# Performance work log

Measured on AMD Instinct MI355X. Metric: run time of the kernel, lower is better.

The kernel has to match this reference:

```python
import jax, jax.numpy as jnp
import numpy as np
from jax import lax

N_FEAT = 150          # feature-map side
N_AR = 9              # anchors per cell
PRE_NMS = 6000        # mode='test'
POST_NMS = 300        # mode='test'
IOU_TH = 0.7
MIN_SIZE = 16.0 / 1000.0


def _make_anchors():
    # grid of centers in [0,1], 9 anchors per cell (3 scales x 3 ratios), xyxy form
    cs = (np.arange(N_FEAT) + 0.5) / N_FEAT
    cy, cx = np.meshgrid(cs, cs, indexing='ij')
    scales = np.array([0.05, 0.1, 0.2])
    ratios = np.array([0.5, 1.0, 2.0])
    ws = (scales[:, None] * np.sqrt(ratios)[None, :]).reshape(-1)  # [9]
    hs = (scales[:, None] / np.sqrt(ratios)[None, :]).reshape(-1)
    cx = np.repeat(cx.reshape(-1), N_AR)
    cy = np.repeat(cy.reshape(-1), N_AR)
    ws = np.tile(ws, N_FEAT * N_FEAT)
    hs = np.tile(hs, N_FEAT * N_FEAT)
    xy = np.stack([cx - ws / 2, cy - hs / 2, cx + ws / 2, cy + hs / 2], axis=-1)
    return xy.astype(np.float32)  # [N,4]


def xy_to_cxcy(xy):
    return jnp.concatenate([(xy[:, 2:] + xy[:, :2]) / 2, xy[:, 2:] - xy[:, :2]], axis=-1)


def cxcy_to_xy(cxcy):
    return jnp.concatenate([cxcy[:, :2] - cxcy[:, 2:] / 2, cxcy[:, :2] + cxcy[:, 2:] / 2], axis=-1)


def decode(t, priors_cxcy):
    cxcy = t[:, :2] * priors_cxcy[:, 2:] + priors_cxcy[:, :2]
    wh = jnp.exp(t[:, 2:]) * priors_cxcy[:, 2:]
    return jnp.concatenate([cxcy, wh], axis=-1)


def pairwise_iou(b):
    # b: [K,4] xyxy -> [K,K]
    area = (b[:, 2] - b[:, 0]) * (b[:, 3] - b[:, 1])
    lt = jnp.maximum(b[:, None, :2], b[None, :, :2])
    rb = jnp.minimum(b[:, None, 2:], b[None, :, 2:])
    wh = jnp.clip(rb - lt, 0.0)
    inter = wh[..., 0] * wh[..., 1]
    return inter / (area[:, None] + area[None, :] - inter + 1e-12)


def greedy_nms_mask(boxes, valid):
    # boxes sorted by score desc; returns bool keep mask of shape [K]
    K = boxes.shape[0]
    iou = pairwise_iou(boxes)  # [K,K]  (~144 MB for K=6000)
    idx = jnp.arange(K)

    def body(i, keep):
        active = keep[i] & valid[i]
        supp = (iou[i] > IOU_TH) & (idx > i) & active
        return keep & ~supp

    keep = lax.fori_loop(0, K, body, jnp.ones(K, dtype=bool))
    return keep & valid


def setup_inputs() -> dict:
    key = jax.random.key(0)
    k1, k2 = jax.random.split(key)
    N = N_FEAT * N_FEAT * N_AR
    pred_cls = jax.random.normal(k1, (1, N, 2), dtype=jnp.float32)
    pred_loc = jax.random.normal(k2, (1, N, 4), dtype=jnp.float32) * 0.1
    anchor = jnp.asarray(_make_anchors())
    return {"pred_cls": pred_cls, "pred_loc": pred_loc, "anchor": anchor}


def reference(pred_cls, pred_loc, anchor):
    # squeeze batch dim of 1
    scores = jax.nn.softmax(pred_cls[0], axis=-1)[:, 1]  # [N] objectness
    priors = xy_to_cxcy(anchor)
    roi = jnp.clip(cxcy_to_xy(decode(pred_loc[0], priors)), 0.0, 1.0)  # [N,4]

    ws = roi[:, 2] - roi[:, 0]
    hs = roi[:, 3] - roi[:, 1]
    valid = (ws >= MIN_SIZE) & (hs >= MIN_SIZE)

    # size filter via masking (scores in [0,1], so -1 sorts below all valid)
    scores_m = jnp.where(valid, scores, -1.0)
    top_scores, top_idx = lax.top_k(scores_m, PRE_NMS)
    boxes = roi[top_idx]           # [PRE_NMS,4], score-descending
    valid_k = top_scores >= 0.0

    keep = greedy_nms_mask(boxes, valid_k)  # [PRE_NMS] bool

    # gather kept boxes in score order, take first POST_NMS, zero-pad the rest
    order = jnp.argsort(jnp.where(keep, jnp.arange(PRE_NMS), PRE_NMS))
    sel = order[:POST_NMS]
    out = boxes[sel] * keep[sel][:, None].astype(boxes.dtype)  # [POST_NMS,4]
    return out
```

## Files before the change

### kernel.cpp

```cpp
#include <hip/hip_runtime.h>
#include <hip/hip_bf16.h>

#define NANCH 202500
#define PRE_NMS 6000
#define POST_NMS 300
#define KW 94
#define CAP 8192
#define NBUCK 16384
#define BSHIFT 18
#define IOU_TH 0.7f
#define MIN_SIZE 0.016f
#define TB_PAD 6016
#define RTILE 256
#define RITEMS 8
#define SBLK 256
#define CBLK 198

typedef unsigned long long ull;

__device__ inline float4 decode_box(const float* __restrict__ loc,
                                    const float* __restrict__ anc, int i) {
    float4 a = ((const float4*)anc)[i];
    float4 t = ((const float4*)loc)[i];
    float pw = a.z - a.x, ph = a.w - a.y;
    float pcx = (a.x + a.z) * 0.5f, pcy = (a.y + a.w) * 0.5f;
    float cx = t.x * pw + pcx, cy = t.y * ph + pcy;
    float w = expf(t.z) * pw, h = expf(t.w) * ph;
    float x1 = fminf(fmaxf(cx - 0.5f * w, 0.f), 1.f);
    float y1 = fminf(fmaxf(cy - 0.5f * h, 0.f), 1.f);
    float x2 = fminf(fmaxf(cx + 0.5f * w, 0.f), 1.f);
    float y2 = fminf(fmaxf(cy + 0.5f * h, 0.f), 1.f);
    return make_float4(x1, y1, x2, y2);
}

__device__ inline unsigned make_key(const float* __restrict__ cls,
                                    const float* __restrict__ loc,
                                    const float* __restrict__ anc, int i) {
    float2 c = ((const float2*)cls)[i];
    float d = c.y - c.x;
    float4 b = decode_box(loc, anc, i);
    bool valid = ((b.z - b.x) >= MIN_SIZE) && ((b.w - b.y) >= MIN_SIZE);
    unsigned ib = __float_as_uint(d);
    unsigned u = (ib & 0x80000000u) ? ~ib : (ib | 0x80000000u);
    return valid ? u : 0u;
}

__device__ inline ull orx64(ull v, int m) {
    unsigned lo = (unsigned)v, hi = (unsigned)(v >> 32);
    lo = (unsigned)__shfl_xor((int)lo, m, 64);
    hi = (unsigned)__shfl_xor((int)hi, m, 64);
    return ((ull)hi << 32) | lo;
}

__device__ inline bool iou_gt(float4 bi, float4 bj, float ai) {
    float aj = (bj.z - bj.x) * (bj.w - bj.y);
    float lx = fmaxf(bi.x, bj.x), ly = fmaxf(bi.y, bj.y);
    float rx = fminf(bi.z, bj.z), ry = fminf(bi.w, bj.w);
    float iw = fmaxf(rx - lx, 0.f), ih = fmaxf(ry - ly, 0.f);
    float inter = iw * ih;
    return inter > IOU_TH * (ai + aj - inter);
}

__global__ __launch_bounds__(256) void k_score(const float* __restrict__ cls,
                                               const float* __restrict__ loc,
                                               const float* __restrict__ anc,
                                               unsigned* __restrict__ hist,
                                               unsigned* __restrict__ keyc, int n) {
    __shared__ unsigned lh[NBUCK];
    int tid = threadIdx.x, bid = blockIdx.x;
    for (int q = tid; q < NBUCK; q += 256) lh[q] = 0u;
    __syncthreads();
    for (int i = bid * 256 + tid; i < n; i += SBLK * 256) {
        unsigned u = make_key(cls, loc, anc, i);
        if (keyc) keyc[i] = u;
        atomicAdd(&lh[u >> BSHIFT], 1u);
    }
    __syncthreads();
    for (int qq = 0; qq < NBUCK / 256; qq++) {
        int q = (qq + bid) & (NBUCK / 256 - 1);
        int b = q * 256 + tid;
        unsigned v = lh[b];
        if (v) atomicAdd(&hist[b], v);
    }
}

__global__ __launch_bounds__(256) void k_compactB(const unsigned* __restrict__ keyc,
                                                  const unsigned* __restrict__ hist,
                                                  unsigned* __restrict__ meta,
                                                  ull* __restrict__ cand, int n) {
    __shared__ unsigned ps[256];
    __shared__ unsigned Bs;
    __shared__ unsigned wbase[5];
    int tid = threadIdx.x, bid = blockIdx.x;
    const uint4* h4 = (const uint4*)hist;
    unsigned local = 0;
    #pragma unroll
    for (int b = 0; b < 16; b++) {
        uint4 v = h4[tid * 16 + b];
        local += v.x + v.y + v.z + v.w;
    }
    ps[tid] = local;
    __syncthreads();
    for (int off = 1; off < 256; off <<= 1) {
        unsigned add = (tid + off < 256) ? ps[tid + off] : 0u;
        __syncthreads();
        ps[tid] += add;
        __syncthreads();
    }
    unsigned incl = ps[tid];
    unsigned excl = incl - local;
    if (incl >= (unsigned)PRE_NMS && excl < (unsigned)PRE_NMS) {
        unsigned hv[64];
        #pragma unroll
        for (int b = 0; b < 16; b++) {
            uint4 v = h4[tid * 16 + b];
            hv[4 * b] = v.x; hv[4 * b + 1] = v.y;
            hv[4 * b + 2] = v.z; hv[4 * b + 3] = v.w;
        }
        unsigned cum = excl;
        int B = tid * 64;
        for (int b = 63; b >= 0; b--) {
            cum += hv[b];
            if (cum >= (unsigned)PRE_NMS) { B = tid * 64 + b; break; }
        }
        Bs = (unsigned)B;
    }
    __syncthreads();
    unsigned B = Bs;
    int lane = tid & 63, wv = tid >> 6;
    unsigned uk[4]; bool pr[4]; unsigned lpre[4], kpre[4];
    ull ltm = (1ull << lane) - 1ull;
    unsigned wsum = 0;
    #pragma unroll
    for (int k = 0; k < 4; k++) {
        int i = bid * 1024 + k * 256 + tid;
        unsigned u = (i < n) ? keyc[i] : 0u;
        uk[k] = u;
        bool pred = (i < n) && ((u >> BSHIFT) >= B);
        pr[k] = pred;
        ull m = __ballot(pred);
        lpre[k] = (unsigned)__popcll(m & ltm);
        kpre[k] = wsum;
        wsum += (unsigned)__popcll(m);
    }
    if (lane == 0) wbase[wv] = wsum;
    __syncthreads();
    if (tid == 0) {
        unsigned s = 0;
        #pragma unroll
        for (int w = 0; w < 4; w++) { unsigned t = wbase[w]; wbase[w] = s; s += t; }
        wbase[4] = atomicAdd(&meta[1], s);
    }
    __syncthreads();
    unsigned base = wbase[4] + wbase[wv];
    #pragma unroll
    for (int k = 0; k < 4; k++) {
        if (pr[k]) {
            unsigned p = base + kpre[k] + lpre[k];
            if (p < CAP)
                cand[p] = ((ull)(~uk[k]) << 32) | (unsigned)(bid * 1024 + k * 256 + tid);
        }
    }
}

__global__ __launch_bounds__(256) void k_ranksc(const ull* __restrict__ cand,
                                                const unsigned* __restrict__ meta,
                                                const float* __restrict__ loc,
                                                const float* __restrict__ anc,
                                                float4* __restrict__ topbox,
                                                ull* __restrict__ vmask) {
    __shared__ __align__(16) ull tile[256];
    int tid = threadIdx.x, bid = blockIdx.x;
    unsigned C = meta[1]; if (C > CAP) C = CAP;
    int sub = tid >> 3, octl = tid & 7;
    int ci = bid * 32 + sub;
    ull ki = (ci < (int)C) ? cand[ci] : 0ull;
    unsigned cnt = 0;
    int ntile = ((int)C + 255) / 256;
    for (int tt = 0; tt < ntile; tt++) {
        int j = tt * 256 + tid;
        tile[tid] = (j < (int)C) ? cand[j] : ~0ull;
        __syncthreads();
        #pragma unroll
        for (int jj = 0; jj < 32; jj++)
            cnt += (unsigned)(tile[jj * 8 + octl] < ki);
        __syncthreads();
    }
    cnt += (unsigned)__shfl_xor((int)cnt, 1, 64);
    cnt += (unsigned)__shfl_xor((int)cnt, 2, 64);
    cnt += (unsigned)__shfl_xor((int)cnt, 4, 64);
    if (octl == 0 && ci < (int)C) {
        unsigned uu = ~(unsigned)(ki >> 32);
        if (uu != 0u && cnt < (unsigned)PRE_NMS) {
            topbox[cnt] = decode_box(loc, anc, (int)(unsigned)ki);
            atomicOr(&vmask[cnt >> 6], 1ull << (cnt & 63));
        }
    }
}

__global__ __launch_bounds__(64) void k_supp(const float4* __restrict__ topbox,
                                             ull* __restrict__ supp,
                                             ull* __restrict__ sdg) {
    int cb = blockIdx.x, rb = blockIdx.y;
    if (cb < rb) return;
    int i = rb * 64 + threadIdx.x;
    __shared__ float4 cbox[64];
    int jt = cb * 64 + threadIdx.x;
    cbox[threadIdx.x] = (jt < PRE_NMS) ? topbox[jt] : make_float4(0.f, 0.f, 0.f, 0.f);
    __syncthreads();
    if (i >= PRE_NMS) return;
    float4 bi = topbox[i];
    float ai = (bi.z - bi.x) * (bi.w - bi.y);
    ull bits = 0ull;
    int j0 = cb * 64;
    for (int jj = 0; jj < 64; jj++) {
        int j = j0 + jj;
        if (j <= i || j >= PRE_NMS) continue;
        if (iou_gt(bi, cbox[jj], ai)) bits |= (1ull << jj);
    }
    supp[(size_t)i * KW + cb] = bits;
    if (cb == rb) sdg[i] = bits;
}

__global__ __launch_bounds__(64) void k_scan(const ull* __restrict__ supp,
                                             const ull* __restrict__ sdg,
                                             const ull* __restrict__ vmask,
                                             const float4* __restrict__ topbox,
                                             float* __restrict__ out) {
    __shared__ int klist[POST_NMS + 64];
    __shared__ ull vm_s[KW];
    int l = threadIdx.x;
    for (int q = l; q < KW; q += 64) vm_s[q] = vmask[q];
    __syncthreads();
    int nk = 0;
    for (int c = 0; c < KW && nk < POST_NMS; c++) {
        ull vm = vm_s[c];
        if (!vm) continue;
        int row = c * 64 + l;
        ull sd = (row < PRE_NMS) ? sdg[row] : 0ull;
        ull inc = 0ull;
        for (int q = l; q < nk; q += 64)
            inc |= supp[(size_t)klist[q] * KW + c];
        #pragma unroll
        for (int off = 32; off; off >>= 1) inc |= orx64(inc, off);
        ull todo = vm & ~inc;
        unsigned tlo = __builtin_amdgcn_readfirstlane((unsigned)todo);
        unsigned thi = __builtin_amdgcn_readfirstlane((unsigned)(todo >> 32));
        ull td = ((ull)thi << 32) | tlo;
        if (!td) continue;
        unsigned sdlo = (unsigned)sd, sdhi = (unsigned)(sd >> 32);
        ull keepw = 0ull;
        while (td) {
            int b = __builtin_ctzll(td);
            unsigned mlo = __builtin_amdgcn_readlane(sdlo, b);
            unsigned mhi = __builtin_amdgcn_readlane(sdhi, b);
            ull m = (((ull)mhi << 32) | mlo) | (1ull << b);
            keepw |= 1ull << b;
            td &= ~m;
        }
        int pos = nk + (int)__popcll(keepw & ((1ull << l) - 1ull));
        if ((keepw >> l) & 1ull) klist[pos] = row;
        nk += (int)__popcll(keepw);
        __syncthreads();
    }
    __syncthreads();
    int nout = nk < POST_NMS ? nk : POST_NMS;
    for (int q = l; q < nout; q += 64)
        ((float4*)out)[q] = topbox[klist[q]];
    for (int q = nout + l; q < POST_NMS; q += 64)
        ((float4*)out)[q] = make_float4(0.f, 0.f, 0.f, 0.f);
}

__global__ __launch_bounds__(1024) void k_findb(const unsigned* __restrict__ hist,
                                                unsigned* __restrict__ meta) {
    __shared__ unsigned ps[1024];
    int t = threadIdx.x;
    int base = t * (NBUCK / 1024);
    unsigned local = 0;
    for (int b = 0; b < NBUCK / 1024; b++) local += hist[base + b];
    ps[t] = local;
    __syncthreads();
    for (int off = 1; off < 1024; off <<= 1) {
        unsigned add = (t + off < 1024) ? ps[t + off] : 0u;
        __syncthreads();
        ps[t] += add;
        __syncthreads();
    }
    unsigned incl = ps[t];
    unsigned excl = incl - local;
    if (incl >= (unsigned)PRE_NMS && excl < (unsigned)PRE_NMS) {
        unsigned cum = excl;
        int B = base;
        for (int b = NBUCK / 1024 - 1; b >= 0; b--) {
            cum += hist[base + b];
            if (cum >= (unsigned)PRE_NMS) { B = base + b; break; }
        }
        meta[0] = (unsigned)B;
    }
}

__global__ __launch_bounds__(256) void k_compactR(const float* __restrict__ cls,
                                                  const float* __restrict__ loc,
                                                  const float* __restrict__ anc,
                                                  unsigned* __restrict__ meta,
                                                  ull* __restrict__ cand, int n) {
    int i = blockIdx.x * blockDim.x + threadIdx.x;
    if (i >= n) return;
    unsigned u = make_key(cls, loc, anc, i);
    if ((u >> BSHIFT) >= meta[0]) {
        unsigned p = atomicAdd(&meta[1], 1u);
        if (p < CAP) cand[p] = ((ull)(~u) << 32) | (unsigned)i;
    }
}

__global__ __launch_bounds__(256) void k_rank(const ull* __restrict__ cand,
                                              const unsigned* __restrict__ meta,
                                              unsigned* __restrict__ rank,
                                              float4* __restrict__ topbox) {
    __shared__ __align__(16) ull tile[RTILE];
    int tid = threadIdx.x;
    int bx = blockIdx.x, by = blockIdx.y;
    unsigned C = meta[1]; if (C > CAP) C = CAP;
    if (by == 0) {
        int per = TB_PAD / (CAP / (256 * RITEMS));
        int s0 = bx * per;
        for (int q = tid; q < per; q += 256)
            topbox[s0 + q] = make_float4(-1.f, -1.f, -1.f, -1.f);
    }
    int ibase = bx * 256 * RITEMS;
    ull ki[RITEMS]; unsigned cnt[RITEMS];
    #pragma unroll
    for (int r = 0; r < RITEMS; r++) {
        int i = ibase + r * 256 + tid;
        ki[r] = (i < (int)C) ? cand[i] : ~0ull;
        cnt[r] = 0u;
    }
    int j = by * RTILE + tid;
    tile[tid] = (j < (int)C) ? cand[j] : ~0ull;
    __syncthreads();
    const ulonglong2* t2 = (const ulonglong2*)tile;
    for (int q = 0; q < RTILE / 2; q++) {
        ulonglong2 v = t2[q];
        #pragma unroll
        for (int r = 0; r < RITEMS; r++)
            cnt[r] += (unsigned)(v.x < ki[r]) + (unsigned)(v.y < ki[r]);
    }
    #pragma unroll
    for (int r = 0; r < RITEMS; r++)
        if (cnt[r]) atomicAdd(&rank[ibase + r * 256 + tid], cnt[r]);
}

__global__ __launch_bounds__(256) void k_scatter(const ull* __restrict__ cand,
                                                 const unsigned* __restrict__ meta,
                                                 const unsigned* __restrict__ rank,
                                                 const float* __restrict__ loc,
                                                 const float* __restrict__ anc,
                                                 float4* __restrict__ topbox,
                                                 ull* __restrict__ vmask) {
    int i = blockIdx.x * 256 + threadIdx.x;
    unsigned C = meta[1]; if (C > CAP) C = CAP;
    if (i >= (int)C) return;
    ull kv = cand[i];
    unsigned uu = ~(unsigned)(kv >> 32);
    if (uu == 0u) return;
    unsigned r = rank[i];
    if (r >= PRE_NMS) return;
    int idx = (int)(unsigned)kv;
    topbox[r] = decode_box(loc, anc, idx);
    atomicOr(&vmask[r >> 6], 1ull << (r & 63));
}

__global__ __launch_bounds__(64) void k_nms(const float4* __restrict__ topbox,
                                            float* __restrict__ out) {
    int l = threadIdx.x;
    float4 kb[5];
    int nk = 0;
    for (int q0 = 0; q0 < TB_PAD && nk < POST_NMS; q0 += 64) {
        float4 myb = topbox[q0 + l];
        for (int b = 0; b < 64 && nk < POST_NMS; b++) {
            float4 bb;
            bb.x = __shfl(myb.x, b, 64);
            bb.y = __shfl(myb.y, b, 64);
            bb.z = __shfl(myb.z, b, 64);
            bb.w = __shfl(myb.w, b, 64);
            if (bb.x < 0.f) continue;
            float ab = (bb.z - bb.x) * (bb.w - bb.y);
            bool sup = false;
            #pragma unroll
            for (int r = 0; r < 5; r++) {
                int s = r * 64 + l;
                if (s < nk) {
                    float4 kv = kb[r];
                    float ak = (kv.z - kv.x) * (kv.w - kv.y);
                    float lx = fmaxf(bb.x, kv.x), ly = fmaxf(bb.y, kv.y);
                    float rx = fminf(bb.z, kv.z), ry = fminf(bb.w, kv.w);
                    float iw = fmaxf(rx - lx, 0.f), ih = fmaxf(ry - ly, 0.f);
                    float inter = iw * ih;
                    float iou = inter / (ab + ak - inter + 1e-12f);
                    sup |= (iou > IOU_TH);
                }
            }
            if (!__any(sup)) {
                if (l == (nk & 63)) kb[nk >> 6] = bb;
                if (l < 4) {
                    float v = (l == 0) ? bb.x : (l == 1) ? bb.y : (l == 2) ? bb.z : bb.w;
                    out[4 * nk + l] = v;
                }
                nk++;
            }
        }
    }
    for (int t = nk * 4 + l; t < POST_NMS * 4; t += 64) out[t] = 0.f;
}

extern "C" void kernel_launch(void* const* d_in, const int* in_sizes, int n_in,
                              void* d_out, int out_size, void* d_ws, size_t ws_size,
                              hipStream_t stream) {
    const int N = in_sizes[0] / 2;
    const float* cls = (const float*)d_in[0];
    const float* loc = (const float*)d_in[1];
    const float* anc = (const float*)d_in[2];
    float* out = (float*)d_out;

    char* ws = (char*)d_ws;
    size_t off = 0;
    auto take = [&](size_t bytes) {
        size_t o = off;
        off += (bytes + 255) & ~(size_t)255;
        return o;
    };
    unsigned* hist = (unsigned*)(ws + take((size_t)NBUCK * 4));
    char*     mblk = ws + take(1024);
    unsigned* meta  = (unsigned*)mblk;
    ull*      vmask = (ull*)(mblk + 256);
    unsigned* rank = (unsigned*)(ws + take((size_t)CAP * 4));
    size_t zlen = off;
    ull*    cand   = (ull*)(ws + take((size_t)CAP * 8));
    float4* topbox = (float4*)(ws + take((size_t)TB_PAD * 16));
    unsigned* keyc = (unsigned*)(ws + take((size_t)N * 4));
    ull*      supp = (ull*)(ws + take((size_t)PRE_NMS * KW * 8));
    ull*      sdg  = (ull*)(ws + take((size_t)TB_PAD * 8));
    size_t full_need = off;
    const bool fast = (ws_size >= full_need);

    hipMemsetAsync(ws, 0, zlen, stream);

    if (fast) {
        k_score<<<SBLK, 256, 0, stream>>>(cls, loc, anc, hist, keyc, N);
        k_compactB<<<CBLK, 256, 0, stream>>>(keyc, hist, meta, cand, N);
        k_ranksc<<<CAP / 32, 256, 0, stream>>>(cand, meta, loc, anc, topbox, vmask);
        k_supp<<<dim3(KW, KW), 64, 0, stream>>>(topbox, supp, sdg);
        k_scan<<<1, 64, 0, stream>>>(supp, sdg, vmask, topbox, out);
    } else {
        dim3 rgrid(CAP / (256 * RITEMS), CAP / RTILE);
        k_score<<<SBLK, 256, 0, stream>>>(cls, loc, anc, hist, (unsigned*)nullptr, N);
        k_findb<<<1, 1024, 0, stream>>>(hist, meta);
        k_compactR<<<(N + 255) / 256, 256, 0, stream>>>(cls, loc, anc, meta, cand, N);
        k_rank<<<rgrid, 256, 0, stream>>>(cand, meta, rank, topbox);
        k_scatter<<<CAP / 256, 256, 0, stream>>>(cand, meta, rank, loc, anc, topbox, vmask);
        k_nms<<<1, 64, 0, stream>>>(topbox, out);
    }
}
```

Measured before the change: 149.5 us.

## Fuse suppression matrix and greedy scan into one kernel with last-block scan

```diff
diff --git a/kernel.cpp b/kernel.cpp
--- a/kernel.cpp
+++ b/kernel.cpp
@@ -15,6 +15,7 @@
 #define RITEMS 8
 #define SBLK 256
 #define CBLK 198
+#define GSUP 16
 
 typedef unsigned long long ull;
 
@@ -198,70 +199,114 @@
     }
 }
 
-__global__ __launch_bounds__(64) void k_supp(const float4* __restrict__ topbox,
-                                             ull* __restrict__ supp,
-                                             ull* __restrict__ sdg) {
-    int cb = blockIdx.x, rb = blockIdx.y;
-    if (cb < rb) return;
-    int i = rb * 64 + threadIdx.x;
+__global__ __launch_bounds__(64) void k_suppscan(const float4* __restrict__ topbox,
+                                                 ull* __restrict__ supp,
+                                                 ull* __restrict__ sdg,
+                                                 const ull* __restrict__ vmask,
+                                                 float* __restrict__ out,
+                                                 unsigned* __restrict__ meta,
+                                                 unsigned* __restrict__ rowc) {
     __shared__ float4 cbox[64];
-    int jt = cb * 64 + threadIdx.x;
-    cbox[threadIdx.x] = (jt < PRE_NMS) ? topbox[jt] : make_float4(0.f, 0.f, 0.f, 0.f);
-    __syncthreads();
-    if (i >= PRE_NMS) return;
-    float4 bi = topbox[i];
-    float ai = (bi.z - bi.x) * (bi.w - bi.y);
-    ull bits = 0ull;
-    int j0 = cb * 64;
-    for (int jj = 0; jj < 64; jj++) {
-        int j = j0 + jj;
-        if (j <= i || j >= PRE_NMS) continue;
-        if (iou_gt(bi, cbox[jj], ai)) bits |= (1ull << jj);
-    }
-    supp[(size_t)i * KW + cb] = bits;
-    if (cb == rb) sdg[i] = bits;
-}
-
-__global__ __launch_bounds__(64) void k_scan(const ull* __restrict__ supp,
-                                             const ull* __restrict__ sdg,
-                                             const ull* __restrict__ vmask,
-                                             const float4* __restrict__ topbox,
-                                             float* __restrict__ out) {
     __shared__ int klist[POST_NMS + 64];
     __shared__ ull vm_s[KW];
-    int l = threadIdx.x;
+    int g = blockIdx.x, rb = blockIdx.y, l = threadIdx.x;
+    int i = rb * 64 + l;
+    bool act = (i < PRE_NMS);
+    float4 bi = act ? topbox[i] : make_float4(0.f, 0.f, 0.f, 0.f);
+    float ai = (bi.z - bi.x) * (bi.w - bi.y);
+    for (int cb = rb + g; cb < KW; cb += GSUP) {
+        int jt = cb * 64 + l;
+        cbox[l] = (jt < PRE_NMS) ? topbox[jt] : make_float4(0.f, 0.f, 0.f, 0.f);
+        __syncthreads();
+        if (act) {
+            ull bits = 0ull;
+            int j0 = cb * 64;
+            for (int jj = 0; jj < 64; jj++) {
+                int j = j0 + jj;
+                if (j <= i || j >= PRE_NMS) continue;
+                if (iou_gt(bi, cbox[jj], ai)) bits |= (1ull << jj);
+            }
+            supp[(size_t)i * KW + cb] = bits;
+            if (cb == rb) sdg[i] = bits;
+        }
+        __syncthreads();
+    }
+    __syncthreads();
+    unsigned amlast = 0;
+    if (l == 0) {
+        __threadfence();
+        if (atomicAdd(&rowc[rb], 1u) == (unsigned)(GSUP - 1))
+            if (atomicAdd(&meta[2], 1u) == (unsigned)(KW - 1))
+                amlast = 1;
+    }
+    amlast = (unsigned)__shfl((int)amlast, 0, 64);
+    if (!amlast) return;
+    __threadfence();
+
     for (int q = l; q < KW; q += 64) vm_s[q] = vmask[q];
+    if (l == 0) klist[0] = 0;
     __syncthreads();
     int nk = 0;
+    ull g0 = 0, g1 = 0, g2 = 0, g3 = 0, g4 = 0, g5 = 0;
+    int nkG = 0;
+    ull sdv = sdg[l];
+    ull snv = supp[(size_t)l * KW + 1];
+    unsigned fslo = 0, fshi = 0;
     for (int c = 0; c < KW && nk < POST_NMS; c++) {
-        ull vm = vm_s[c];
-        if (!vm) continue;
-        int row = c * 64 + l;
-        ull sd = (row < PRE_NMS) ? sdg[row] : 0ull;
-        ull inc = 0ull;
-        for (int q = l; q < nk; q += 64)
-            inc |= supp[(size_t)klist[q] * KW + c];
+        ull pgv = 0;
+        if (l       < nkG) pgv |= g0;
+        if (l +  64 < nkG) pgv |= g1;
+        if (l + 128 < nkG) pgv |= g2;
+        if (l + 192 < nkG) pgv |= g3;
+        if (l + 256 < nkG) pgv |= g4;
+        if (l + 320 < nkG) pgv |= g5;
         #pragma unroll
-        for (int off = 32; off; off >>= 1) inc |= orx64(inc, off);
-        ull todo = vm & ~inc;
-        unsigned tlo = __builtin_amdgcn_readfirstlane((unsigned)todo);
-        unsigned thi = __builtin_amdgcn_readfirstlane((unsigned)(todo >> 32));
+        for (int off = 32; off; off >>= 1) pgv |= orx64(pgv, off);
+        ull tdv = vm_s[c] & ~pgv;
+        unsigned tlo = __builtin_amdgcn_readfirstlane((unsigned)tdv) & ~fslo;
+        unsigned thi = __builtin_amdgcn_readfirstlane((unsigned)(tdv >> 32)) & ~fshi;
         ull td = ((ull)thi << 32) | tlo;
-        if (!td) continue;
-        unsigned sdlo = (unsigned)sd, sdhi = (unsigned)(sd >> 32);
-        ull keepw = 0ull;
-        while (td) {
-            int b = __builtin_ctzll(td);
-            unsigned mlo = __builtin_amdgcn_readlane(sdlo, b);
-            unsigned mhi = __builtin_amdgcn_readlane(sdhi, b);
-            ull m = (((ull)mhi << 32) | mlo) | (1ull << b);
-            keepw |= 1ull << b;
-            td &= ~m;
-        }
-        int pos = nk + (int)__popcll(keepw & ((1ull << l) - 1ull));
-        if ((keepw >> l) & 1ull) klist[pos] = row;
-        nk += (int)__popcll(keepw);
-        __syncthreads();
+        int cn = (c + 1 < KW) ? c + 1 : KW - 1;
+        int nm1 = (nk > 0) ? nk - 1 : 0;
+        int q0 = (l       < nk) ? l       : nm1;
+        int q1 = (l +  64 < nk) ? l +  64 : nm1;
+        int q2 = (l + 128 < nk) ? l + 128 : nm1;
+        int q3 = (l + 192 < nk) ? l + 192 : nm1;
+        int q4 = (l + 256 < nk) ? l + 256 : nm1;
+        int q5 = (l + 320 < nk) ? l + 320 : nm1;
+        g0 = supp[(size_t)klist[q0] * KW + cn];
+        g1 = supp[(size_t)klist[q1] * KW + cn];
+        g2 = supp[(size_t)klist[q2] * KW + cn];
+        g3 = supp[(size_t)klist[q3] * KW + cn];
+        g4 = supp[(size_t)klist[q4] * KW + cn];
+        g5 = supp[(size_t)klist[q5] * KW + cn];
+        nkG = nk;
+        int rn = cn * 64 + l;
+        ull sdn = sdg[(rn < TB_PAD) ? rn : TB_PAD - 1];
+        int rn2 = (rn < PRE_NMS) ? rn : PRE_NMS - 1;
+        int cn2 = (c + 2 < KW) ? c + 2 : KW - 1;
+        ull snn = supp[(size_t)rn2 * KW + cn2];
+        unsigned nfslo = 0, nfshi = 0;
+        if (td) {
+            unsigned sdlo = (unsigned)sdv, sdhi = (unsigned)(sdv >> 32);
+            unsigned snlo = (unsigned)snv, snhi = (unsigned)(snv >> 32);
+            ull keepw = 0ull;
+            while (td) {
+                int b = __builtin_ctzll(td);
+                unsigned mlo = __builtin_amdgcn_readlane(sdlo, b);
+                unsigned mhi = __builtin_amdgcn_readlane(sdhi, b);
+                nfslo |= __builtin_amdgcn_readlane(snlo, b);
+                nfshi |= __builtin_amdgcn_readlane(snhi, b);
+                ull m = (((ull)mhi << 32) | mlo) | (1ull << b);
+                keepw |= 1ull << b;
+                td &= ~m;
+            }
+            int pos = nk + (int)__popcll(keepw & ((1ull << l) - 1ull));
+            if ((keepw >> l) & 1ull) klist[pos] = c * 64 + l;
+            nk += (int)__popcll(keepw);
+        }
+        fslo = nfslo; fshi = nfshi;
+        sdv = sdn; snv = snn;
     }
     __syncthreads();
     int nout = nk < POST_NMS ? nk : POST_NMS;
@@ -430,9 +475,10 @@
         return o;
     };
     unsigned* hist = (unsigned*)(ws + take((size_t)NBUCK * 4));
-    char*     mblk = ws + take(1024);
+    char*     mblk = ws + take(2048);
     unsigned* meta  = (unsigned*)mblk;
     ull*      vmask = (ull*)(mblk + 256);
+    unsigned* rowc  = (unsigned*)(mblk + 1024);
     unsigned* rank = (unsigned*)(ws + take((size_t)CAP * 4));
     size_t zlen = off;
     ull*    cand   = (ull*)(ws + take((size_t)CAP * 8));
@@ -449,8 +495,7 @@
         k_score<<<SBLK, 256, 0, stream>>>(cls, loc, anc, hist, keyc, N);
         k_compactB<<<CBLK, 256, 0, stream>>>(keyc, hist, meta, cand, N);
         k_ranksc<<<CAP / 32, 256, 0, stream>>>(cand, meta, loc, anc, topbox, vmask);
-        k_supp<<<dim3(KW, KW), 64, 0, stream>>>(topbox, supp, sdg);
-        k_scan<<<1, 64, 0, stream>>>(supp, sdg, vmask, topbox, out);
+        k_suppscan<<<dim3(GSUP, KW), 64, 0, stream>>>(topbox, supp, sdg, vmask, out, meta, rowc);
     } else {
         dim3 rgrid(CAP / (256 * RITEMS), CAP / RTILE);
         k_score<<<SBLK, 256, 0, stream>>>(cls, loc, anc, hist, (unsigned*)nullptr, N);
```

New measurement: 201.4 us. +34.7%, slower.
